# Kernel optimization log

Measured on AMD Instinct MI355X. Metric: run time of the kernel, lower is better.

Reference implementation:

```python
import jax, jax.numpy as jnp
import numpy as np

B, A, M, C = 8, 49104, 50, 90
ALPHA, GAMMA = 0.25, 2.0


def _calc_iou(a, b):
    # a: [A,4] anchors in (y1,x1,y2,x2); b: [M,4] boxes in (x1,y1,x2,y2)
    area = (b[:, 2] - b[:, 0]) * (b[:, 3] - b[:, 1])                      # [M]
    iw = jnp.minimum(a[:, 3:4], b[None, :, 2]) - jnp.maximum(a[:, 1:2], b[None, :, 0])
    ih = jnp.minimum(a[:, 2:3], b[None, :, 3]) - jnp.maximum(a[:, 0:1], b[None, :, 1])
    iw = jnp.clip(iw, 0.0)
    ih = jnp.clip(ih, 0.0)
    a_area = (a[:, 2] - a[:, 0]) * (a[:, 3] - a[:, 1])                    # [A]
    ua = jnp.clip(a_area[:, None] + area[None, :] - iw * ih, 1e-8)
    return iw * ih / ua                                                    # [A,M]


def _per_sample(classification, regression, box, label, anchor, aw, ah, acx, acy):
    valid = label != 0
    lab = jnp.where(valid, label - 1, 0)                                   # shift: 0 is padding
    iou = _calc_iou(anchor, box)                                           # [A,M]
    iou = jnp.where(valid[None, :], iou, -1.0)                             # mask padded GT
    iou_max = iou.max(axis=1)
    iou_arg = iou.argmax(axis=1)
    assigned = box[iou_arg]                                                # [A,4] xyxy
    alab = lab[iou_arg]                                                    # [A]
    big = (assigned[:, 2] - assigned[:, 0]) * (assigned[:, 3] - assigned[:, 1]) > 100.0
    pos = (big & (iou_max >= 0.5)) | (~big & (iou_max >= 0.15))            # [A] bool
    num_pos = pos.sum()

    cls = jnp.clip(classification, 1e-4, 1.0 - 1e-4)
    targets = jax.nn.one_hot(alab, cls.shape[1], dtype=cls.dtype) * pos[:, None].astype(cls.dtype)
    alpha_factor = jnp.where(targets == 1.0, ALPHA, 1.0 - ALPHA)
    focal_weight = jnp.where(targets == 1.0, 1.0 - cls, cls)
    bce = -(targets * jnp.log(cls) + (1.0 - targets) * jnp.log(1.0 - cls))
    cls_loss = (alpha_factor * focal_weight ** GAMMA * bce).sum() / jnp.maximum(num_pos.astype(cls.dtype), 1.0)

    gw0 = assigned[:, 2] - assigned[:, 0]
    gh0 = assigned[:, 3] - assigned[:, 1]
    gcx = assigned[:, 0] + 0.5 * gw0
    gcy = assigned[:, 1] + 0.5 * gh0
    gw = jnp.clip(gw0, 1.0)
    gh = jnp.clip(gh0, 1.0)
    tdx = (gcx - acx) / aw
    tdy = (gcy - acy) / ah
    tdw = jnp.log(gw / aw)
    tdh = jnp.log(gh / ah)
    tgt = jnp.stack([tdy, tdx, tdh, tdw], axis=-1)                         # [A,4]
    diff = jnp.abs(tgt - regression)
    sl1 = jnp.where(diff <= 1.0 / 9.0, 0.5 * 9.0 * diff ** 2, diff - 0.5 / 9.0)
    reg_sum = (sl1 * pos[:, None].astype(sl1.dtype)).sum()
    npos = jnp.maximum(num_pos, 1).astype(sl1.dtype)
    reg_loss = jnp.where(num_pos > 0, reg_sum / (npos * 4.0), 0.0)
    return cls_loss, reg_loss


def setup_inputs() -> dict:
    key = jax.random.key(0)
    ka1, ka2, ka3, ka4, kb, kc, kr = jax.random.split(key, 7)
    # anchors in (y1,x1,y2,x2)
    cy = jax.random.uniform(ka1, (A,)) * 512.0
    cx = jax.random.uniform(ka2, (A,)) * 512.0
    h = 8.0 + jax.random.uniform(ka3, (A,)) * 120.0
    w = 8.0 + jax.random.uniform(ka4, (A,)) * 120.0
    anchors = jnp.stack([cy - 0.5 * h, cx - 0.5 * w, cy + 0.5 * h, cx + 0.5 * w], axis=-1)[None]
    # GT boxes in (x1,y1,x2,y2)
    kx, ky, kw, kh, kl = jax.random.split(kb, 5)
    x1 = jax.random.uniform(kx, (B, M)) * 400.0
    y1 = jax.random.uniform(ky, (B, M)) * 400.0
    bw = 5.0 + jax.random.uniform(kw, (B, M)) * 100.0
    bh = 5.0 + jax.random.uniform(kh, (B, M)) * 100.0
    detection_boxes = jnp.stack([x1, y1, x1 + bw, y1 + bh], axis=-1)
    detection_labels = jax.random.randint(kl, (B, M), 0, C + 1, dtype=jnp.int32)  # 0 = padding
    classification = jax.random.uniform(kc, (B, A, C), minval=0.01, maxval=0.99)
    regression = jax.random.normal(kr, (B, A, 4)) * 0.1
    return {"detection_boxes": detection_boxes, "detection_labels": detection_labels,
            "regression": regression, "classification": classification, "anchors": anchors}


def reference(detection_boxes, detection_labels, regression, classification, anchors):
    anchor = anchors[0]
    aw = anchor[:, 3] - anchor[:, 1]
    ah = anchor[:, 2] - anchor[:, 0]
    acx = anchor[:, 1] + 0.5 * aw
    acy = anchor[:, 0] + 0.5 * ah
    cls_l, reg_l = jax.vmap(_per_sample, in_axes=(0, 0, 0, 0, None, None, None, None, None))(
        classification, regression, detection_boxes, detection_labels, anchor, aw, ah, acx, acy)
    cls_loss = cls_l.mean(axis=0, keepdims=True)
    det_loss = reg_l.mean(axis=0, keepdims=True) * 50.0
    return (cls_loss, det_loss)
```

## Files before the change

kernel.cpp:

```cpp
#include <hip/hip_runtime.h>
#include <cmath>

#define NB 8
#define NA 49104
#define NM 50
#define NC 90
#define NBLK 192


__device__ __forceinline__ float clipc(float x) {
    return fminf(fmaxf(x, 1e-4f), 1.0f - 1e-4f);
}

__device__ __forceinline__ float negterm(float x) {
    const float c = clipc(x);
    return 0.75f * c * c * (-__logf(1.0f - c));
}

__device__ __forceinline__ float block_reduce(float v, float* red) {
#pragma unroll
    for (int o = 32; o > 0; o >>= 1) v += __shfl_down(v, o, 64);
    const int wave = threadIdx.x >> 6;
    const int lane = threadIdx.x & 63;
    if (lane == 0) red[wave] = v;
    __syncthreads();
    float r = 0.f;
    if (threadIdx.x == 0) {
        const int nw = blockDim.x >> 6;
        for (int w = 0; w < nw; ++w) r += red[w];
    }
    __syncthreads();
    return r;
}

__global__ __launch_bounds__(256) void fused_kernel(
    const float* __restrict__ boxes,
    const int*   __restrict__ labels,
    const float* __restrict__ regression,
    const float* __restrict__ cls,
    const float* __restrict__ anchors,
    float* __restrict__ ws) {
    __shared__ float4 sbox[NM];
    __shared__ float  sarea[NM];
    __shared__ int    slab[NM];
    __shared__ float  red[4];

    const int b  = blockIdx.y;
    const int t  = threadIdx.x;
    const int a0 = blockIdx.x << 8;

    if (t < NM) {
        float4 bx = ((const float4*)boxes)[b * NM + t];
        const int l = labels[b * NM + t];
        float area = (bx.z - bx.x) * (bx.w - bx.y);
        if (l == 0) {
            bx.x = bx.y = bx.z = bx.w = 3e38f;
            area = 0.f;
        }
        sbox[t]  = bx;
        sarea[t] = area;
        slab[t]  = (l != 0) ? (l - 1) : 0;
    }
    __syncthreads();

    float corr = 0.f, regs = 0.f, npos = 0.f;
    const int a = a0 + t;
    if (a < NA) {
        const float4 an = ((const float4*)anchors)[a];
        const float ay1 = an.x, ax1 = an.y, ay2 = an.z, ax2 = an.w;
        const float aarea = (ay2 - ay1) * (ax2 - ax1);

        float best = -1.f;
        int arg = 0;
        for (int m = 0; m < NM; ++m) {
            const float4 bx = sbox[m];
            float iw = fminf(ax2, bx.z) - fmaxf(ax1, bx.x);
            float ih = fminf(ay2, bx.w) - fmaxf(ay1, bx.y);
            iw = fmaxf(iw, 0.f);
            ih = fmaxf(ih, 0.f);
            const float inter = iw * ih;
            const float ua = fmaxf(aarea + sarea[m] - inter, 1e-8f);
            const float iou = inter / ua;
            if (iou > best) { best = iou; arg = m; }
        }

        const bool big = sarea[arg] > 100.0f;
        const bool pos = big ? (best >= 0.5f) : (best >= 0.15f);
        if (pos) {
            npos = 1.f;
            const float4 bx = sbox[arg];
            const float aw = ax2 - ax1, ah = ay2 - ay1;
            const float acx = ax1 + 0.5f * aw, acy = ay1 + 0.5f * ah;
            const float gw0 = bx.z - bx.x, gh0 = bx.w - bx.y;
            const float gcx = bx.x + 0.5f * gw0, gcy = bx.y + 0.5f * gh0;
            const float gw = fmaxf(gw0, 1.f), gh = fmaxf(gh0, 1.f);
            const float4 r = ((const float4*)regression)[b * NA + a];
            const float d0 = fabsf((gcy - acy) / ah - r.x);
            const float d1 = fabsf((gcx - acx) / aw - r.y);
            const float d2 = fabsf(__logf(gh / ah) - r.z);
            const float d3 = fabsf(__logf(gw / aw) - r.w);
            regs  = (d0 <= 1.f / 9.f) ? 4.5f * d0 * d0 : d0 - (0.5f / 9.f);
            regs += (d1 <= 1.f / 9.f) ? 4.5f * d1 * d1 : d1 - (0.5f / 9.f);
            regs += (d2 <= 1.f / 9.f) ? 4.5f * d2 * d2 : d2 - (0.5f / 9.f);
            regs += (d3 <= 1.f / 9.f) ? 4.5f * d3 * d3 : d3 - (0.5f / 9.f);

            const int alab = slab[arg];
            const float c = clipc(cls[((size_t)b * NA + a) * NC + alab]);
            const float omc = 1.f - c;
            corr = 0.25f * omc * omc * (-__logf(c)) -
                   0.75f * c * c * (-__logf(omc));
        }
    }

    const int aend = (a0 + 256 < NA) ? a0 + 256 : NA;
    const int n4 = ((aend - a0) * NC) >> 2;
    const float4* p = (const float4*)(cls + ((size_t)b * NA + a0) * NC);
    float neg = 0.f;
    for (int i = t; i < n4; i += 256) {
        const float4 v = p[i];
        neg += negterm(v.x) + negterm(v.y) + negterm(v.z) + negterm(v.w);
    }

    const float tc = block_reduce(neg + corr, red);
    const float tr = block_reduce(regs, red);
    const float tn = block_reduce(npos, red);
    if (t == 0) {
        const int idx = b * NBLK + blockIdx.x;
        ws[idx]                 = tc;
        ws[NB * NBLK + idx]     = tr;
        ws[2 * NB * NBLK + idx] = tn;
    }
}

__global__ __launch_bounds__(256) void finalize_kernel(
    const float* __restrict__ ws, float* __restrict__ out) {
    __shared__ float red[4];
    const int t = threadIdx.x;
    float cl = 0.f, rl = 0.f;
    for (int b = 0; b < NB; ++b) {
        const float vc = (t < NBLK) ? ws[b * NBLK + t] : 0.f;
        const float vr = (t < NBLK) ? ws[NB * NBLK + b * NBLK + t] : 0.f;
        const float vn = (t < NBLK) ? ws[2 * NB * NBLK + b * NBLK + t] : 0.f;
        const float sc = block_reduce(vc, red);
        const float sr = block_reduce(vr, red);
        const float sn = block_reduce(vn, red);
        if (t == 0) {
            cl += sc / fmaxf(sn, 1.f);
            rl += (sn > 0.f) ? sr / (sn * 4.f) : 0.f;
        }
    }
    if (t == 0) {
        out[0] = cl / (float)NB;
        out[1] = rl / (float)NB * 50.f;
    }
}

extern "C" void kernel_launch(void* const* d_in, const int* in_sizes, int n_in,
                              void* d_out, int out_size, void* d_ws,
                              size_t ws_size, hipStream_t stream) {
    const float* boxes      = (const float*)d_in[0];
    const int*   labels     = (const int*)d_in[1];
    const float* regression = (const float*)d_in[2];
    const float* cls        = (const float*)d_in[3];
    const float* anchors    = (const float*)d_in[4];
    float* out = (float*)d_out;
    float* ws  = (float*)d_ws;

    dim3 g(NBLK, NB);
    fused_kernel<<<g, 256, 0, stream>>>(boxes, labels, regression, cls,
                                        anchors, ws);
    finalize_kernel<<<1, 256, 0, stream>>>(ws, out);
}
```

Measured before the change: 235.4 us.

## Fuse finalize into main kernel via cooperative grid sync, enlarge per-block anchor range

Replaces the two-kernel scheme with a single cooperative launch: each block now handles 384 anchors in a strided loop (128 blocks per batch, 1024 total), writes its partials, then a grid-wide sync lets block (0,0) perform the final reduction. This removes the second kernel launch and its dependency gap, and reduces the number of blocks. The cost is a grid barrier and fewer, longer-running blocks, which may reduce latency hiding for the memory-bound classification stream. Co-residency of all 1024 blocks is required for the cooperative launch to succeed.

```diff
diff --git a/kernel.cpp b/kernel.cpp
--- a/kernel.cpp
+++ b/kernel.cpp
@@ -1,11 +1,15 @@
 #include <hip/hip_runtime.h>
+#include <hip/hip_cooperative_groups.h>
 #include <cmath>
+
+namespace cg = cooperative_groups;
 
 #define NB 8
 #define NA 49104
 #define NM 50
 #define NC 90
-#define NBLK 192
+#define NBX 128
+#define APB 384
 
 
 __device__ __forceinline__ float clipc(float x) {
@@ -33,13 +37,14 @@
     return r;
 }
 
-__global__ __launch_bounds__(256) void fused_kernel(
+__global__ __launch_bounds__(256, 4) void fused_kernel(
     const float* __restrict__ boxes,
     const int*   __restrict__ labels,
     const float* __restrict__ regression,
     const float* __restrict__ cls,
     const float* __restrict__ anchors,
-    float* __restrict__ ws) {
+    float* __restrict__ ws,
+    float* __restrict__ out) {
     __shared__ float4 sbox[NM];
     __shared__ float  sarea[NM];
     __shared__ int    slab[NM];
@@ -47,7 +52,8 @@
 
     const int b  = blockIdx.y;
     const int t  = threadIdx.x;
-    const int a0 = blockIdx.x << 8;
+    const int a0 = blockIdx.x * APB;
+    const int aend = (a0 + APB < NA) ? a0 + APB : NA;
 
     if (t < NM) {
         float4 bx = ((const float4*)boxes)[b * NM + t];
@@ -64,8 +70,7 @@
     __syncthreads();
 
     float corr = 0.f, regs = 0.f, npos = 0.f;
-    const int a = a0 + t;
-    if (a < NA) {
+    for (int a = a0 + t; a < aend; a += 256) {
         const float4 an = ((const float4*)anchors)[a];
         const float ay1 = an.x, ax1 = an.y, ay2 = an.z, ax2 = an.w;
         const float aarea = (ay2 - ay1) * (ax2 - ax1);
@@ -87,7 +92,7 @@
         const bool big = sarea[arg] > 100.0f;
         const bool pos = big ? (best >= 0.5f) : (best >= 0.15f);
         if (pos) {
-            npos = 1.f;
+            npos += 1.f;
             const float4 bx = sbox[arg];
             const float aw = ax2 - ax1, ah = ay2 - ay1;
             const float acx = ax1 + 0.5f * aw, acy = ay1 + 0.5f * ah;
@@ -99,7 +104,7 @@
             const float d1 = fabsf((gcx - acx) / aw - r.y);
             const float d2 = fabsf(__logf(gh / ah) - r.z);
             const float d3 = fabsf(__logf(gw / aw) - r.w);
-            regs  = (d0 <= 1.f / 9.f) ? 4.5f * d0 * d0 : d0 - (0.5f / 9.f);
+            regs += (d0 <= 1.f / 9.f) ? 4.5f * d0 * d0 : d0 - (0.5f / 9.f);
             regs += (d1 <= 1.f / 9.f) ? 4.5f * d1 * d1 : d1 - (0.5f / 9.f);
             regs += (d2 <= 1.f / 9.f) ? 4.5f * d2 * d2 : d2 - (0.5f / 9.f);
             regs += (d3 <= 1.f / 9.f) ? 4.5f * d3 * d3 : d3 - (0.5f / 9.f);
@@ -107,12 +112,11 @@
             const int alab = slab[arg];
             const float c = clipc(cls[((size_t)b * NA + a) * NC + alab]);
             const float omc = 1.f - c;
-            corr = 0.25f * omc * omc * (-__logf(c)) -
-                   0.75f * c * c * (-__logf(omc));
+            corr += 0.25f * omc * omc * (-__logf(c)) -
+                    0.75f * c * c * (-__logf(omc));
         }
     }
 
-    const int aend = (a0 + 256 < NA) ? a0 + 256 : NA;
     const int n4 = ((aend - a0) * NC) >> 2;
     const float4* p = (const float4*)(cls + ((size_t)b * NA + a0) * NC);
     float neg = 0.f;
@@ -125,22 +129,21 @@
     const float tr = block_reduce(regs, red);
     const float tn = block_reduce(npos, red);
     if (t == 0) {
-        const int idx = b * NBLK + blockIdx.x;
-        ws[idx]                 = tc;
-        ws[NB * NBLK + idx]     = tr;
-        ws[2 * NB * NBLK + idx] = tn;
+        const int idx = b * NBX + blockIdx.x;
+        ws[idx]                = tc;
+        ws[NB * NBX + idx]     = tr;
+        ws[2 * NB * NBX + idx] = tn;
     }
-}
+    __threadfence();
 
-__global__ __launch_bounds__(256) void finalize_kernel(
-    const float* __restrict__ ws, float* __restrict__ out) {
-    __shared__ float red[4];
-    const int t = threadIdx.x;
+    cg::this_grid().sync();
+
+    if (blockIdx.x != 0 || blockIdx.y != 0) return;
     float cl = 0.f, rl = 0.f;
-    for (int b = 0; b < NB; ++b) {
-        const float vc = (t < NBLK) ? ws[b * NBLK + t] : 0.f;
-        const float vr = (t < NBLK) ? ws[NB * NBLK + b * NBLK + t] : 0.f;
-        const float vn = (t < NBLK) ? ws[2 * NB * NBLK + b * NBLK + t] : 0.f;
+    for (int bb = 0; bb < NB; ++bb) {
+        const float vc = (t < NBX) ? ws[bb * NBX + t] : 0.f;
+        const float vr = (t < NBX) ? ws[NB * NBX + bb * NBX + t] : 0.f;
+        const float vn = (t < NBX) ? ws[2 * NB * NBX + bb * NBX + t] : 0.f;
         const float sc = block_reduce(vc, red);
         const float sr = block_reduce(vr, red);
         const float sn = block_reduce(vn, red);
@@ -166,8 +169,8 @@
     float* out = (float*)d_out;
     float* ws  = (float*)d_ws;
 
-    dim3 g(NBLK, NB);
-    fused_kernel<<<g, 256, 0, stream>>>(boxes, labels, regression, cls,
-                                        anchors, ws);
-    finalize_kernel<<<1, 256, 0, stream>>>(ws, out);
+    void* args[] = {(void*)&boxes, (void*)&labels, (void*)&regression,
+                    (void*)&cls,   (void*)&anchors, (void*)&ws, (void*)&out};
+    hipLaunchCooperativeKernel((const void*)fused_kernel,
+                               dim3(NBX, NB), dim3(256), args, 0, stream);
 }
```

Result: slower. 463.4 us (+96.8%).
